# Kernel optimization log

Measured on AMD Instinct MI355X. Metric: run time of the kernel, lower is better.

Reference implementation:

```python
import jax, jax.numpy as jnp
import numpy as np

V, E, H, B, S, T = 32000, 512, 1024, 32, 64, 64

def setup_inputs() -> dict:
    key = jax.random.key(0)
    ks = jax.random.split(key, 26)
    p = 0.02  # param init scale
    inp = {
        "enc_h": jax.random.normal(ks[0], (B, S, 2 * H), dtype=jnp.float32),
        "prev_s": jax.random.normal(ks[1], (B, H), dtype=jnp.float32),
        "target": jax.random.randint(ks[2], (B, T), 0, V, dtype=jnp.int32),
        "embed": jax.random.normal(ks[3], (V, E), dtype=jnp.float32) * p,
        # Attention params
        "att_Wenc": jax.random.normal(ks[4], (2 * H, H), dtype=jnp.float32) * p,
        "att_benc": jnp.zeros((H,), dtype=jnp.float32),
        "att_Wprev": jax.random.normal(ks[5], (H, H), dtype=jnp.float32) * p,
        "att_bprev": jnp.zeros((H,), dtype=jnp.float32),
        "att_wlin": jax.random.normal(ks[6], (H, 1), dtype=jnp.float32) * p,
        "att_blin": jnp.zeros((1,), dtype=jnp.float32),
        # DecoderCell gate params (input/hidden/ctx -> 2H)
        "dc_Wi": jax.random.normal(ks[7], (E, 2 * H), dtype=jnp.float32) * p,
        "dc_bi": jnp.zeros((2 * H,), dtype=jnp.float32),
        "dc_Wh": jax.random.normal(ks[8], (H, 2 * H), dtype=jnp.float32) * p,
        "dc_bh": jnp.zeros((2 * H,), dtype=jnp.float32),
        "dc_Wc": jax.random.normal(ks[9], (2 * H, 2 * H), dtype=jnp.float32) * p,
        "dc_bc": jnp.zeros((2 * H,), dtype=jnp.float32),
        # DecoderCell candidate params (-> H)
        "dc_Wi2": jax.random.normal(ks[10], (E, H), dtype=jnp.float32) * p,
        "dc_bi2": jnp.zeros((H,), dtype=jnp.float32),
        "dc_Wh2": jax.random.normal(ks[11], (H, H), dtype=jnp.float32) * p,
        "dc_bh2": jnp.zeros((H,), dtype=jnp.float32),
        "dc_Wc2": jax.random.normal(ks[12], (2 * H, H), dtype=jnp.float32) * p,
        "dc_bc2": jnp.zeros((H,), dtype=jnp.float32),
        # dec2word
        "out_W": jax.random.normal(ks[13], (H, V), dtype=jnp.float32) * p,
        "out_b": jnp.zeros((V,), dtype=jnp.float32),
    }
    return inp


def reference(enc_h, prev_s, target, embed, att_Wenc, att_benc, att_Wprev,
              att_bprev, att_wlin, att_blin, dc_Wi, dc_bi, dc_Wh, dc_bh,
              dc_Wc, dc_bc, dc_Wi2, dc_bi2, dc_Wh2, dc_bh2, dc_Wc2, dc_bc2,
              out_W, out_b):
    h = prev_s.shape[-1]
    # Precompute attention key projection (weights fixed across timesteps)
    enc_proj = enc_h @ att_Wenc + att_benc          # B x S x H
    xs = jnp.transpose(embed[target], (1, 0, 2))    # T x B x E

    def step(s_prev, x_t):
        # Bahdanau attention
        q = s_prev @ att_Wprev + att_bprev                       # B x H
        score = jnp.tanh(enc_proj + q[:, None, :]) @ att_wlin + att_blin  # B x S x 1
        alpha = jax.nn.softmax(score[..., 0], axis=1)            # B x S (over seq)
        ctx = jnp.einsum('bs,bsh->bh', alpha, enc_h)             # B x 2H
        # GRU-like cell (original uses only the first chunk of gates)
        gates = (x_t @ dc_Wi + dc_bi) + (s_prev @ dc_Wh + dc_bh) + (ctx @ dc_Wc + dc_bc)
        reset = jax.nn.sigmoid(gates[:, :h])
        s_tilde = jnp.tanh((x_t @ dc_Wi2 + dc_bi2) + (s_prev @ dc_Wh2 + dc_bh2) + (ctx @ dc_Wc2 + dc_bc2))
        s_new = (1.0 - reset) * s_prev + reset * s_tilde
        return s_new, s_new

    final_s, dec_h = jax.lax.scan(step, prev_s, xs)   # dec_h: T x B x H
    outputs = jnp.transpose(dec_h, (1, 0, 2)) @ out_W + out_b  # B x T x V
    return outputs, final_s
```

## Files before the change

kernel.cpp:

```cpp
#include <hip/hip_runtime.h>

#define B_   32
#define S_   64
#define T_   64
#define H_   1024
#define H2_  2048
#define E_   512
#define V_   32000
#define K3_  3072
#define BT_  2048

typedef unsigned short u16;
typedef __attribute__((ext_vector_type(8))) short short8_t;
typedef __attribute__((ext_vector_type(4))) float f32x4;

__device__ __forceinline__ u16 f2bf(float f) {
  unsigned x = __float_as_uint(f);
  unsigned r = (x + 0x7fffu + ((x >> 16) & 1u)) >> 16;
  return (u16)r;
}
__device__ __forceinline__ float bf2f(u16 h) {
  return __uint_as_float(((unsigned)h) << 16);
}
__device__ __forceinline__ float frcp(float x) { return __builtin_amdgcn_rcpf(x); }
__device__ __forceinline__ float ftanh(float x) {
  float e = __expf(2.f * x);
  return 1.f - 2.f * frcp(e + 1.f);
}
__device__ __forceinline__ float fsigm(float x) {
  return frcp(1.f + __expf(-x));
}

#define KEEPV(x) asm volatile("" : "+v"(x))

__device__ __forceinline__ void st_u16(u16* p, u16 v) {
  __hip_atomic_store(p, v, __ATOMIC_RELAXED, __HIP_MEMORY_SCOPE_AGENT);
}
__device__ __forceinline__ void st_f32(float* p, float v) {
  __hip_atomic_store(p, v, __ATOMIC_RELAXED, __HIP_MEMORY_SCOPE_AGENT);
}

#define MB_ (1ull << 20)
#define KB_ (1ull << 10)
#define X_OFF    (0)
#define SPP_OFF  (0)
#define XGR_OFF  (4*MB_)
#define XG2_OFF  (12*MB_)
#define ENCT_OFF (20*MB_)
#define XCV_OFF  (20*MB_)
#define ENCP_OFF (28*MB_)
#define W2_OFF   (36*MB_)
#define WGF_OFF  (38*MB_)
#define XSV_OFF  (38*MB_)
#define DECH_OFF (46*MB_)
#define WOT_OFF  (0)
#define XS0_OFF  (62*MB_)
#define MB_OFF   (62*MB_ + 128*KB_)
#define BAR_OFF  (62*MB_ + 256*KB_)
#define WLB_OFF  (62*MB_ + 272*KB_)
#define BCR_OFF  (62*MB_ + 276*KB_)
#define BC2_OFF  (62*MB_ + 280*KB_)

__device__ __forceinline__ u16* xs_hi(char* w, int t) {
  return (u16*)(t == 0 ? (w + XS0_OFF) : (w + XSV_OFF + (size_t)(t - 1) * 131072));
}
__device__ __forceinline__ u16* xc_hi(char* w, int t) {
  return (u16*)(w + XCV_OFF + (size_t)t * 262144);
}
__device__ __forceinline__ float* spp_v(char* w, int t) {
  return (float*)(w + SPP_OFF + (size_t)t * 65536);
}

__device__ void gemm_body(char* smemRaw,
                          const float* __restrict__ A, int lda,
                          const float* __restrict__ Bm, int ldb,
                          void* __restrict__ Cv, int ldc, int outBf16,
                          const float* __restrict__ bias, const float* __restrict__ bias2,
                          int mtiles, int ntiles, int K, int bid) {
  u16 (*As)[72] = (u16(*)[72])smemRaw;
  u16 (*Bs)[72] = (u16(*)[72])(smemRaw + 128 * 72 * 2);
  int nwg = mtiles * ntiles;
  int cpx = nwg >> 3;
  int lb = (bid & 7) * cpx + (bid >> 3);
  int ntb = lb / mtiles, mtb = lb - ntb * mtiles;
  size_t m0 = (size_t)mtb * 128, n0 = (size_t)ntb * 128;
  int t = threadIdx.x, lane = t & 63, wid = t >> 6;
  int wr = (wid >> 1) * 64, wc = (wid & 1) * 64;
  f32x4 acc[4][4] = {};
  for (int k0 = 0; k0 < K; k0 += 64) {
    #pragma unroll
    for (int i = 0; i < 8; ++i) {
      int f4 = i * 256 + t;
      int row = f4 >> 4, c4 = (f4 & 15) << 2;
      float4 v = *(const float4*)(A + (m0 + row) * (size_t)lda + k0 + c4);
      ushort4 u; u.x = f2bf(v.x); u.y = f2bf(v.y); u.z = f2bf(v.z); u.w = f2bf(v.w);
      *(ushort4*)&As[row][c4] = u;
    }
    #pragma unroll
    for (int i = 0; i < 8; ++i) {
      int f4 = i * 256 + t;
      int kr = f4 >> 5, c4 = (f4 & 31) << 2;
      float4 v = *(const float4*)(Bm + (size_t)(k0 + kr) * ldb + n0 + c4);
      Bs[c4 + 0][kr] = f2bf(v.x);
      Bs[c4 + 1][kr] = f2bf(v.y);
      Bs[c4 + 2][kr] = f2bf(v.z);
      Bs[c4 + 3][kr] = f2bf(v.w);
    }
    __syncthreads();
    #pragma unroll
    for (int kk = 0; kk < 64; kk += 32) {
      int ko = kk + (lane >> 4) * 8;
      short8_t am[4], bn[4];
      #pragma unroll
      for (int m = 0; m < 4; ++m) am[m] = *(const short8_t*)&As[wr + m * 16 + (lane & 15)][ko];
      #pragma unroll
      for (int n = 0; n < 4; ++n) bn[n] = *(const short8_t*)&Bs[wc + n * 16 + (lane & 15)][ko];
      #pragma unroll
      for (int m = 0; m < 4; ++m)
        #pragma unroll
        for (int n = 0; n < 4; ++n)
          acc[m][n] = __builtin_amdgcn_mfma_f32_16x16x32_bf16(am[m], bn[n], acc[m][n], 0, 0, 0);
    }
    __syncthreads();
  }
  #pragma unroll
  for (int n = 0; n < 4; ++n) {
    int col = wc + n * 16 + (lane & 15);
    float bv = bias ? bias[n0 + col] : 0.f;
    if (bias2) bv += bias2[n0 + col];
    #pragma unroll
    for (int m = 0; m < 4; ++m) {
      size_t row = m0 + wr + m * 16 + ((lane >> 4) << 2);
      #pragma unroll
      for (int r = 0; r < 4; ++r) {
        float val = acc[m][n][r] + bv;
        if (outBf16) ((u16*)Cv)[(row + r) * (size_t)ldc + n0 + col] = f2bf(val);
        else ((float*)Cv)[(row + r) * (size_t)ldc + n0 + col] = val;
      }
    }
  }
}

__global__ __launch_bounds__(256) void k_prep(
    float* __restrict__ x, const float* __restrict__ embed, const int* __restrict__ tgt,
    u16* __restrict__ encT, const float* __restrict__ enc_h,
    u16* __restrict__ w2, const float* __restrict__ Wprev,
    u16* __restrict__ wgf, const float* __restrict__ Wh, const float* __restrict__ Wc,
    const float* __restrict__ Wh2, const float* __restrict__ Wc2,
    u16* __restrict__ encp, const float* __restrict__ Wenc,
    const float* __restrict__ benc, const float* __restrict__ bprev,
    float* __restrict__ bcr, float* __restrict__ bc2o, u16* __restrict__ wlb,
    const float* __restrict__ bi, const float* __restrict__ bh, const float* __restrict__ bc,
    const float* __restrict__ bi2, const float* __restrict__ bh2, const float* __restrict__ bc2i,
    const float* __restrict__ wlin) {
  __shared__ char pbuf[36864];
  const int bid = blockIdx.x, t = threadIdx.x;

  if (bid < 1024) {
    int f4id = bid * 256 + t;
    int row = f4id >> 7, c4 = f4id & 127;
    int tt = row >> 5, bbb = row & 31;
    int trow = tgt[bbb * T_ + tt];
    ((float4*)x)[(size_t)row * 128 + c4] = ((const float4*)embed)[(size_t)trow * 128 + c4];
  } else if (bid < 2048) {
    u16 (*ld)[68] = (u16(*)[68])pbuf;
    int teb = bid - 1024;
    int b = teb >> 5, et = teb & 31;
    int e0 = et * 64;
    #pragma unroll
    for (int i = 0; i < 4; ++i) {
      int f4 = i * 256 + t;
      int si = f4 >> 4, e4 = (f4 & 15) << 2;
      float4 v = *(const float4*)(enc_h + ((size_t)(b * 64 + si)) * H2_ + e0 + e4);
      ld[si][e4 + 0] = f2bf(v.x); ld[si][e4 + 1] = f2bf(v.y);
      ld[si][e4 + 2] = f2bf(v.z); ld[si][e4 + 3] = f2bf(v.w);
    }
    __syncthreads();
    #pragma unroll
    for (int i = 0; i < 2; ++i) {
      int idx = i * 256 + t;
      int e = idx >> 3, s8 = (idx & 7) << 3;
      short8_t o;
      #pragma unroll
      for (int k = 0; k < 8; ++k) o[k] = (short)ld[s8 + k][e];
      *(short8_t*)(encT + ((size_t)(e0 + e)) * 2048 + b * 64 + s8) = o;
    }
  } else if (bid < 2560) {
    float (*ld)[33] = (float(*)[33])pbuf;
    int pb = bid - 2048;
    int kt = pb >> 5, jt = pb & 31;
    int k0 = kt * 64, j0 = jt * 32;
    #pragma unroll
    for (int i = 0; i < 8; ++i) {
      int idx = i * 256 + t; int kr = idx >> 5, jc = idx & 31;
      ld[kr][jc] = Wprev[(size_t)(k0 + kr) * H_ + j0 + jc];
    }
    __syncthreads();
    int jloc = t >> 3, kk8 = t & 7;
    int j = j0 + jloc;
    int eg = j >> 7;
    int th = ((j & 127) << 2) | (kt >> 2);
    int i = ((kt & 3) << 3) | kk8;
    short8_t o;
    #pragma unroll
    for (int e = 0; e < 8; ++e) o[e] = (short)f2bf(ld[kk8 * 8 + e][jloc]);
    *(short8_t*)(w2 + ((size_t)((eg * 512 + th) * 32 + i)) * 8) = o;
  } else if (bid < 5632) {
    float (*ld)[33] = (float(*)[33])pbuf;
    int pgb = bid - 2560;
    int sel = pgb & 1;
    int jt  = (pgb >> 1) & 31;
    int kt  = pgb >> 6;
    int k0 = kt * 64, j0 = jt * 32;
    const float* srcW = (k0 < H_) ? (sel ? Wh2 : Wh) : (sel ? Wc2 : Wc);
    int ldw = sel ? H_ : H2_;
    int koff = (k0 < H_) ? k0 : (k0 - H_);
    #pragma unroll
    for (int i = 0; i < 8; ++i) {
      int idx = i * 256 + t; int kr = idx >> 5, jc = idx & 31;
      ld[kr][jc] = srcW[(size_t)(koff + kr) * ldw + j0 + jc];
    }
    __syncthreads();
    #pragma unroll
    for (int it = 0; it < 2; ++it) {
      int u = it * 256 + t;
      int m = u & 3, sub = (u >> 2) & 3, kbl = (u >> 4) & 1, islo = (u >> 5) & 1, gg = u >> 6;
      int jjLoc = gg * 4 + m;
      int p = 2 * (j0 + jjLoc) + sel;
      int g = p >> 3, cc = p & 7;
      int c = cc + 8 * islo;
      int KB = kt * 2 + kbl;
      size_t lin = ((size_t)(g * 96 + KB) * 4 + sub) * 16 + c;
      short8_t o;
      #pragma unroll
      for (int j = 0; j < 8; ++j) {
        float v = ld[kbl * 32 + sub * 8 + j][jjLoc];
        u16 h = f2bf(v);
        o[j] = (short)(islo ? f2bf(v - bf2f(h)) : h);
      }
      *(short8_t*)(wgf + lin * 8) = o;
    }
  } else if (bid < 5760) {
    gemm_body(pbuf, enc_h, H2_, Wenc, H_, encp, H_, 1, benc, bprev, 16, 8, H2_, bid - 5632);
  } else {
    int j = (bid - 5760) * 256 + t;
    if (j < H_) {
      bcr[j]  = bi[j]  + bh[j]  + bc[j];
      bc2o[j] = bi2[j] + bh2[j] + bc2i[j];
      wlb[j]  = f2bf(wlin[j]);
    }
  }
}

__global__ __launch_bounds__(256) void k_gemm12(
    const float* __restrict__ x,
    const float* __restrict__ Wi, const float* __restrict__ Wi2,
    float* __restrict__ xgr, float* __restrict__ xg2,
    const float* __restrict__ bcr, const float* __restrict__ bc2) {
  __shared__ char pbuf[36864];
  if (blockIdx.x < 128)
    gemm_body(pbuf, x, E_, Wi, H2_, xgr, H_, 0, bcr, nullptr, 16, 8, E_, blockIdx.x);
  else
    gemm_body(pbuf, x, E_, Wi2, H_, xg2, H_, 0, bc2, nullptr, 16, 8, E_, blockIdx.x - 128);
}

__global__ __launch_bounds__(256) void k_wtrans(u16* __restrict__ wot,
                                                const float* __restrict__ W, int nbase) {
  __shared__ u16 ld[64][68];
  int nt = blockIdx.x % 250, kt = blockIdx.x / 250;
  int n0 = nbase + nt * 64, k0 = kt * 64;
  int t = threadIdx.x;
  #pragma unroll
  for (int i = 0; i < 4; ++i) {
    int f4 = i * 256 + t;
    int kr = f4 >> 4, n4 = (f4 & 15) << 2;
    float4 v = *(const float4*)(W + (size_t)(k0 + kr) * V_ + n0 + n4);
    ld[kr][n4 + 0] = f2bf(v.x); ld[kr][n4 + 1] = f2bf(v.y);
    ld[kr][n4 + 2] = f2bf(v.z); ld[kr][n4 + 3] = f2bf(v.w);
  }
  __syncthreads();
  #pragma unroll
  for (int i = 0; i < 2; ++i) {
    int idx = i * 256 + t;
    int n = idx >> 3, k8 = (idx & 7) << 3;
    short8_t o;
    #pragma unroll
    for (int k = 0; k < 8; ++k) o[k] = (short)ld[k8 + k][n];
    *(short8_t*)(wot + ((size_t)(nt * 64 + n)) * H_ + k0 + k8) = o;
  }
}

__global__ __launch_bounds__(256) void k_gemm2(
    const u16* __restrict__ A, const u16* __restrict__ Bt,
    float* __restrict__ C, const float* __restrict__ bias, int n0g) {
  __shared__ u16 As[128][72];
  __shared__ u16 Bs[128][72];
  int bid = blockIdx.x;
  int lb = (bid & 7) * 250 + (bid >> 3);
  int mtb = lb & 15, ntb = lb >> 4;
  size_t m0 = (size_t)mtb * 128;
  size_t nl0 = (size_t)ntb * 128;
  int t = threadIdx.x, lane = t & 63, wid = t >> 6;
  int wr = (wid >> 1) * 64, wc = (wid & 1) * 64;
  f32x4 acc[4][4] = {};
  for (int k0 = 0; k0 < H_; k0 += 64) {
    #pragma unroll
    for (int i = 0; i < 4; ++i) {
      int idx = i * 256 + t;
      int row = idx >> 3, c8 = (idx & 7) << 3;
      *(short8_t*)&As[row][c8] = *(const short8_t*)(A + (m0 + row) * H_ + k0 + c8);
      *(short8_t*)&Bs[row][c8] = *(const short8_t*)(Bt + (nl0 + row) * H_ + k0 + c8);
    }
    __syncthreads();
    #pragma unroll
    for (int kk = 0; kk < 64; kk += 32) {
      int ko = kk + (lane >> 4) * 8;
      short8_t am[4], bn[4];
      #pragma unroll
      for (int m = 0; m < 4; ++m) am[m] = *(const short8_t*)&As[wr + m * 16 + (lane & 15)][ko];
      #pragma unroll
      for (int n = 0; n < 4; ++n) bn[n] = *(const short8_t*)&Bs[wc + n * 16 + (lane & 15)][ko];
      #pragma unroll
      for (int m = 0; m < 4; ++m)
        #pragma unroll
        for (int n = 0; n < 4; ++n)
          acc[m][n] = __builtin_amdgcn_mfma_f32_16x16x32_bf16(am[m], bn[n], acc[m][n], 0, 0, 0);
    }
    __syncthreads();
  }
  #pragma unroll
  for (int n = 0; n < 4; ++n) {
    int col = n0g + (int)nl0 + wc + n * 16 + (lane & 15);
    float bv = bias[col];
    #pragma unroll
    for (int m = 0; m < 4; ++m) {
      size_t row = m0 + wr + m * 16 + ((lane >> 4) << 2);
      #pragma unroll
      for (int r = 0; r < 4; ++r)
        C[(row + r) * (size_t)V_ + col] = acc[m][n][r] + bv;
    }
  }
}


__device__ __forceinline__ void gridbar(int* bar, int target) {
  asm volatile("s_waitcnt vmcnt(0)" ::: "memory");
  __syncthreads();
  if (threadIdx.x == 0) {
    int* leafcnt = bar;
    int* root    = bar + 512;
    int* leafep  = bar + 768;
    int li = blockIdx.x >> 3;
    if (__hip_atomic_fetch_add(&leafcnt[li * 16], 1, __ATOMIC_RELAXED, __HIP_MEMORY_SCOPE_AGENT) == 7) {
      __hip_atomic_store(&leafcnt[li * 16], 0, __ATOMIC_RELAXED, __HIP_MEMORY_SCOPE_AGENT);
      if (__hip_atomic_fetch_add(root, 1, __ATOMIC_RELAXED, __HIP_MEMORY_SCOPE_AGENT) == 31) {
        __hip_atomic_store(root, 0, __ATOMIC_RELAXED, __HIP_MEMORY_SCOPE_AGENT);
        #pragma unroll
        for (int i = 0; i < 32; ++i)
          __hip_atomic_store(&leafep[i * 16], target, __ATOMIC_RELAXED, __HIP_MEMORY_SCOPE_AGENT);
      }
    }
    while (__hip_atomic_load(&leafep[li * 16], __ATOMIC_RELAXED, __HIP_MEMORY_SCOPE_AGENT) != target)
      __builtin_amdgcn_s_sleep(2);
  }
  __syncthreads();
}

#define MFMA16(a, b, c) __builtin_amdgcn_mfma_f32_16x16x32_bf16((a), (b), (c), 0, 0, 0)

__global__ __launch_bounds__(512, 1) void k_mega(
    char* w, u16* __restrict__ dech, float* __restrict__ fout,
    const u16* __restrict__ w2, const u16* __restrict__ wgf,
    const u16* __restrict__ encp, const u16* __restrict__ encT,
    const float* __restrict__ xgr, const float* __restrict__ xg2,
    const float* __restrict__ prev_s, const u16* __restrict__ wlb,
    int* bar, int* mb) {
  const int t = threadIdx.x, blk = blockIdx.x;
  const int lane = t & 63, wid = t >> 6;
  const int l15 = lane & 15, l4 = lane >> 4;
  const int klo = l4 * 8;
  __shared__ short8_t wg_lds[6144];
  __shared__ f32x4 scr[1024];
  __shared__ float sc[64];
  __shared__ u16 sL[1024];
  __shared__ float qL[8 * 17];
  int ep = 0;

  for (int i = t; i < 6144; i += 512)
    wg_lds[i] = *(const short8_t*)(wgf + ((size_t)blk * 6144 + i) * 8);

  const int bb = blk >> 3, eg = blk & 7;

  const int si_a = t >> 3, jg = t & 7;
  short8_t epv2[2], wlv2[2];
  {
    const u16* p = encp + ((size_t)(bb * 64 + si_a)) * H_ + eg * 128 + jg * 16;
    epv2[0] = *(const short8_t*)(p);     KEEPV(epv2[0]);
    epv2[1] = *(const short8_t*)(p + 8); KEEPV(epv2[1]);
    const u16* q = wlb + eg * 128 + jg * 16;
    wlv2[0] = *(const short8_t*)(q);     KEEPV(wlv2[0]);
    wlv2[1] = *(const short8_t*)(q + 8); KEEPV(wlv2[1]);
  }
  const int eloc = t >> 1, half = t & 1;
  const int ecol = eg * 256 + eloc;
  short8_t et[4];
  #pragma unroll
  for (int i = 0; i < 4; ++i) {
    et[i] = *(const short8_t*)(encT + (size_t)ecol * 2048 + bb * 64 + half * 32 + i * 8);
    KEEPV(et[i]);
  }

  const int pc4 = blk * 8 + l15, jcol = pc4 >> 1, isc = pc4 & 1;
  const int rb = wid * 16 + l4 * 4;
  const bool fin = (wid < 2) && (l15 < 8);
  float sreg[4] = {0.f, 0.f, 0.f, 0.f};

  {
    int idx = blk * 512 + t;
    u16* xs0h = xs_hi(w, 0);
    u16* xs0l = xs0h + B_ * H_;
    if (idx < B_ * H_) {
      float v = prev_s[idx];
      u16 h = f2bf(v);
      st_u16(&xs0h[idx], h);
      st_u16(&xs0l[idx], f2bf(v - bf2f(h)));
    }
    if (fin) {
      #pragma unroll
      for (int r = 0; r < 4; ++r) sreg[r] = prev_s[(rb + r) * H_ + jcol];
    }
  }
  gridbar(bar, ++ep);

  for (int ts = 0; ts < T_; ++ts) {
    const u16* xsh = xs_hi(w, ts);
    const u16* xsl = xsh + B_ * H_;
    u16* xch = xc_hi(w, ts);
    u16* xcl = xch + B_ * H2_;
    float* spp = spp_v(w, ts);
    int* mbp = mb + (ts * 32 + bb) * 16;

    if (t < 128)
      *(short8_t*)&sL[t * 8] = *(const short8_t*)(xsh + bb * H_ + t * 8);
    float xv[4] = {0.f, 0.f, 0.f, 0.f};
    if (fin) {
      const float* xg = isc ? xg2 : xgr;
      #pragma unroll
      for (int r = 0; r < 4; ++r)
        xv[r] = xg[((size_t)ts * B_ + rb + r) * H_ + jcol];
    }
    short8_t pA[4], pB[4], loA[4], loB[4];
    #pragma unroll
    for (int i = 0; i < 4; ++i) {
      int k = (wid + 8 * i) * 32 + klo;
      pA[i]  = *(const short8_t*)(xsh + l15 * H_ + k);        KEEPV(pA[i]);
      pB[i]  = *(const short8_t*)(xsh + (l15 + 16) * H_ + k); KEEPV(pB[i]);
      loA[i] = *(const short8_t*)(xsl + l15 * H_ + k);        KEEPV(loA[i]);
      loB[i] = *(const short8_t*)(xsl + (l15 + 16) * H_ + k); KEEPV(loB[i]);
    }
    __syncthreads();

    {
      const int rot = (t & 3) * 2;
      float qa = 0.f;
      const u16* wp = w2 + ((size_t)(eg * 512 + t)) * 256;
      const u16* sp = sL + (t & 3) * 256;
      #pragma unroll
      for (int i = 0; i < 32; ++i) {
        int ii = (i + rot) & 31;
        short8_t wv = *(const short8_t*)(wp + ii * 8);
        short8_t sv = *(const short8_t*)(sp + ii * 8);
        #pragma unroll
        for (int e = 0; e < 8; ++e)
          qa += bf2f((u16)wv[e]) * bf2f((u16)sv[e]);
      }
      qa += __shfl_xor(qa, 1, 64);
      qa += __shfl_xor(qa, 2, 64);
      if ((t & 3) == 0) { int j = t >> 2; qL[(j >> 4) * 17 + (j & 15)] = qa; }
    }
    __syncthreads();

    {
      float p = 0.f;
      #pragma unroll
      for (int jj = 0; jj < 16; ++jj) {
        float qv = qL[jg * 17 + jj];
        p += ftanh(bf2f((u16)epv2[jj >> 3][jj & 7]) + qv) * bf2f((u16)wlv2[jj >> 3][jj & 7]);
      }
      p += __shfl_xor(p, 1, 64);
      p += __shfl_xor(p, 2, 64);
      p += __shfl_xor(p, 4, 64);
      if (jg == 0) st_f32(&spp[(bb * 64 + si_a) * 8 + eg], p);
    }
    asm volatile("s_waitcnt vmcnt(0)" ::: "memory");
    __syncthreads();
    if (t == 0)
      __hip_atomic_fetch_add(mbp, 1, __ATOMIC_RELAXED, __HIP_MEMORY_SCOPE_AGENT);

    f32x4 aA = {}, aB = {};
    #pragma unroll
    for (int i = 0; i < 4; ++i) {
      short8_t bv = wg_lds[(wid + 8 * i) * 64 + lane];
      aA = MFMA16(pA[i],  bv, aA);
      aB = MFMA16(pB[i],  bv, aB);
      aA = MFMA16(loA[i], bv, aA);
      aB = MFMA16(loB[i], bv, aB);
    }

    if (t == 0) {
      while (__hip_atomic_load(mbp, __ATOMIC_RELAXED, __HIP_MEMORY_SCOPE_AGENT) != 8)
        __builtin_amdgcn_s_sleep(1);
    }
    __syncthreads();

    if (wid == 0) {
      const float* pp = spp + ((size_t)(bb * 64 + lane)) * 8;
      float4 a0 = *(const float4*)(pp);
      float4 a1 = *(const float4*)(pp + 4);
      float v = (a0.x + a0.y + a0.z + a0.w) + (a1.x + a1.y + a1.z + a1.w);
      float m = v;
      #pragma unroll
      for (int off = 32; off; off >>= 1) m = fmaxf(m, __shfl_xor(m, off, 64));
      float e = __expf(v - m);
      float s = e;
      #pragma unroll
      for (int off = 32; off; off >>= 1) s += __shfl_xor(s, off, 64);
      sc[lane] = e * frcp(s);
    }
    __syncthreads();
    {
      float a = 0.f;
      #pragma unroll
      for (int i = 0; i < 4; ++i)
        #pragma unroll
        for (int j = 0; j < 8; ++j)
          a += sc[half * 32 + i * 8 + j] * bf2f((u16)et[i][j]);
      a += __shfl_xor(a, 1, 64);
      if (half == 0) {
        u16 hh = f2bf(a);
        st_u16(&xch[bb * H2_ + ecol], hh);
        st_u16(&xcl[bb * H2_ + ecol], f2bf(a - bf2f(hh)));
      }
    }
    gridbar(bar, ++ep);

    {
      #pragma unroll
      for (int i = 4; i < 12; ++i) {
        int kb = wid + 8 * i;
        int k = kb * 32 + klo - H_;
        short8_t hA = *(const short8_t*)(xch + l15 * H2_ + k);
        short8_t lA = *(const short8_t*)(xcl + l15 * H2_ + k);
        short8_t hB = *(const short8_t*)(xch + (l15 + 16) * H2_ + k);
        short8_t lB = *(const short8_t*)(xcl + (l15 + 16) * H2_ + k);
        short8_t bv = wg_lds[kb * 64 + lane];
        aA = MFMA16(hA, bv, aA);
        aA = MFMA16(lA, bv, aA);
        aB = MFMA16(hB, bv, aB);
        aB = MFMA16(lB, bv, aB);
      }
      scr[(wid * 2 + 0) * 64 + lane] = aA;
      scr[(wid * 2 + 1) * 64 + lane] = aB;
      __syncthreads();
      if (wid < 2) {
        f32x4 s = scr[wid * 64 + lane];
        #pragma unroll
        for (int i = 1; i < 8; ++i) s += scr[(i * 2 + wid) * 64 + lane];
        float tot[4];
        #pragma unroll
        for (int r = 0; r < 4; ++r) tot[r] = s[r] + __shfl_xor(s[r], 8, 64);
        if (l15 < 8) {
          u16* nsh = xs_hi(w, ts + 1);
          u16* nsl = nsh + B_ * H_;
          #pragma unroll
          for (int r = 0; r < 4; ++r) {
            int brow = rb + r;
            float pre = tot[r] + xv[r];
            float mate = __shfl_xor(pre, 1, 64);
            float rpre = isc ? mate : pre;
            float cpre = isc ? pre : mate;
            float rg = fsigm(rpre);
            float cg = ftanh(cpre);
            float sp = sreg[r];
            float sn = sp + rg * (cg - sp);
            sreg[r] = sn;
            if (!isc) {
              u16 hh = f2bf(sn);
              st_u16(&nsh[brow * H_ + jcol], hh);
              st_u16(&nsl[brow * H_ + jcol], f2bf(sn - bf2f(hh)));
              dech[((size_t)brow * T_ + ts) * H_ + jcol] = hh;
              if (ts == T_ - 1) fout[brow * H_ + jcol] = sn;
            }
          }
        }
      }
    }
    gridbar(bar, ++ep);
  }
}


extern "C" void kernel_launch(void* const* d_in, const int* in_sizes, int n_in,
                              void* d_out, int out_size, void* d_ws, size_t ws_size,
                              hipStream_t stream) {
  const float* enc_h    = (const float*)d_in[0];
  const float* prev_s   = (const float*)d_in[1];
  const int*   target   = (const int*)d_in[2];
  const float* embed    = (const float*)d_in[3];
  const float* att_Wenc = (const float*)d_in[4];
  const float* att_benc = (const float*)d_in[5];
  const float* att_Wprev= (const float*)d_in[6];
  const float* att_bprev= (const float*)d_in[7];
  const float* att_wlin = (const float*)d_in[8];
  const float* dc_Wi    = (const float*)d_in[10];
  const float* dc_bi    = (const float*)d_in[11];
  const float* dc_Wh    = (const float*)d_in[12];
  const float* dc_bh    = (const float*)d_in[13];
  const float* dc_Wc    = (const float*)d_in[14];
  const float* dc_bc    = (const float*)d_in[15];
  const float* dc_Wi2   = (const float*)d_in[16];
  const float* dc_bi2   = (const float*)d_in[17];
  const float* dc_Wh2   = (const float*)d_in[18];
  const float* dc_bh2   = (const float*)d_in[19];
  const float* dc_Wc2   = (const float*)d_in[20];
  const float* dc_bc2   = (const float*)d_in[21];
  const float* out_W    = (const float*)d_in[22];
  const float* out_b    = (const float*)d_in[23];

  char* w = (char*)d_ws;
  float* x    = (float*)(w + X_OFF);
  float* xgr  = (float*)(w + XGR_OFF);
  float* xg2  = (float*)(w + XG2_OFF);
  u16*  encT  = (u16*)(w + ENCT_OFF);
  u16*  encp  = (u16*)(w + ENCP_OFF);
  u16*  w2    = (u16*)(w + W2_OFF);
  u16*  wgf   = (u16*)(w + WGF_OFF);
  u16*  wot   = (u16*)(w + WOT_OFF);
  u16*  dech  = (u16*)(w + DECH_OFF);
  u16*  wlb   = (u16*)(w + WLB_OFF);
  float* bcr  = (float*)(w + BCR_OFF);
  float* bc2  = (float*)(w + BC2_OFF);
  int*  bar   = (int*)(w + BAR_OFF);
  int*  mb    = (int*)(w + MB_OFF);
  float* fout = (float*)d_out + (size_t)BT_ * V_;

  hipMemsetAsync(w + MB_OFF, 0, 136 * KB_, stream);

  k_prep<<<5764, 256, 0, stream>>>(x, embed, target, encT, enc_h,
                                   w2, att_Wprev, wgf, dc_Wh, dc_Wc, dc_Wh2, dc_Wc2,
                                   encp, att_Wenc, att_benc, att_bprev,
                                   bcr, bc2, wlb,
                                   dc_bi, dc_bh, dc_bc, dc_bi2, dc_bh2, dc_bc2, att_wlin);
  k_gemm12<<<256, 256, 0, stream>>>(x, dc_Wi, dc_Wi2, xgr, xg2, bcr, bc2);

  k_mega<<<256, 512, 0, stream>>>(w, dech, fout,
                                  w2, wgf, encp, encT, xgr, xg2,
                                  prev_s, wlb, bar, mb);

  k_wtrans<<<4000, 256, 0, stream>>>(wot, out_W, 0);
  k_gemm2 <<<2000, 256, 0, stream>>>(dech, wot, (float*)d_out, out_b, 0);
  k_wtrans<<<4000, 256, 0, stream>>>(wot, out_W, 16000);
  k_gemm2 <<<2000, 256, 0, stream>>>(dech, wot, (float*)d_out, out_b, 16000);
}
```

Baseline: 2.799 ms.

## Fuse output weight transpose and bf16 conversion into vocab GEMM

Removes the separate weight transpose/convert kernels and the bf16 staging buffer, having the output GEMM load fp32 out_W tiles directly, convert to bf16 and transpose through LDS before MFMA. This eliminates a large intermediate write and read and several launches, but each M-tile now re-reads fp32 weights, doubling per-tile weight bytes and adding an LDS transpose stage and extra barrier per k-step. Also skips the final grid barrier after the last recurrent step.

```diff
diff --git a/kernel.cpp b/kernel.cpp
--- a/kernel.cpp
+++ b/kernel.cpp
@@ -53,7 +53,6 @@
 #define WGF_OFF  (38*MB_)
 #define XSV_OFF  (38*MB_)
 #define DECH_OFF (46*MB_)
-#define WOT_OFF  (0)
 #define XS0_OFF  (62*MB_)
 #define MB_OFF   (62*MB_ + 128*KB_)
 #define BAR_OFF  (62*MB_ + 256*KB_)
@@ -264,42 +263,17 @@
     gemm_body(pbuf, x, E_, Wi2, H_, xg2, H_, 0, bc2, nullptr, 16, 8, E_, blockIdx.x - 128);
 }
 
-__global__ __launch_bounds__(256) void k_wtrans(u16* __restrict__ wot,
-                                                const float* __restrict__ W, int nbase) {
-  __shared__ u16 ld[64][68];
-  int nt = blockIdx.x % 250, kt = blockIdx.x / 250;
-  int n0 = nbase + nt * 64, k0 = kt * 64;
-  int t = threadIdx.x;
-  #pragma unroll
-  for (int i = 0; i < 4; ++i) {
-    int f4 = i * 256 + t;
-    int kr = f4 >> 4, n4 = (f4 & 15) << 2;
-    float4 v = *(const float4*)(W + (size_t)(k0 + kr) * V_ + n0 + n4);
-    ld[kr][n4 + 0] = f2bf(v.x); ld[kr][n4 + 1] = f2bf(v.y);
-    ld[kr][n4 + 2] = f2bf(v.z); ld[kr][n4 + 3] = f2bf(v.w);
-  }
-  __syncthreads();
-  #pragma unroll
-  for (int i = 0; i < 2; ++i) {
-    int idx = i * 256 + t;
-    int n = idx >> 3, k8 = (idx & 7) << 3;
-    short8_t o;
-    #pragma unroll
-    for (int k = 0; k < 8; ++k) o[k] = (short)ld[k8 + k][n];
-    *(short8_t*)(wot + ((size_t)(nt * 64 + n)) * H_ + k0 + k8) = o;
-  }
-}
-
-__global__ __launch_bounds__(256) void k_gemm2(
-    const u16* __restrict__ A, const u16* __restrict__ Bt,
-    float* __restrict__ C, const float* __restrict__ bias, int n0g) {
+__global__ __launch_bounds__(256) void k_gemm2d(
+    const u16* __restrict__ A, const float* __restrict__ W,
+    float* __restrict__ C, const float* __restrict__ bias) {
   __shared__ u16 As[128][72];
   __shared__ u16 Bs[128][72];
+  __shared__ u16 Bstage[64 * 132];
   int bid = blockIdx.x;
-  int lb = (bid & 7) * 250 + (bid >> 3);
+  int lb = (bid & 7) * 500 + (bid >> 3);
   int mtb = lb & 15, ntb = lb >> 4;
   size_t m0 = (size_t)mtb * 128;
-  size_t nl0 = (size_t)ntb * 128;
+  size_t n0 = (size_t)ntb * 128;
   int t = threadIdx.x, lane = t & 63, wid = t >> 6;
   int wr = (wid >> 1) * 64, wc = (wid & 1) * 64;
   f32x4 acc[4][4] = {};
@@ -309,7 +283,24 @@
       int idx = i * 256 + t;
       int row = idx >> 3, c8 = (idx & 7) << 3;
       *(short8_t*)&As[row][c8] = *(const short8_t*)(A + (m0 + row) * H_ + k0 + c8);
-      *(short8_t*)&Bs[row][c8] = *(const short8_t*)(Bt + (nl0 + row) * H_ + k0 + c8);
+    }
+    #pragma unroll
+    for (int i = 0; i < 8; ++i) {
+      int f4 = i * 256 + t;
+      int kr = f4 >> 5, c4 = (f4 & 31) << 2;
+      float4 v = *(const float4*)(W + (size_t)(k0 + kr) * V_ + n0 + c4);
+      ushort4 u; u.x = f2bf(v.x); u.y = f2bf(v.y); u.z = f2bf(v.z); u.w = f2bf(v.w);
+      *(ushort4*)&Bstage[kr * 132 + c4] = u;
+    }
+    __syncthreads();
+    #pragma unroll
+    for (int i = 0; i < 4; ++i) {
+      int jj = i * 256 + t;
+      int n = jj & 127, k8 = jj >> 7;
+      short8_t o;
+      #pragma unroll
+      for (int e = 0; e < 8; ++e) o[e] = (short)Bstage[(k8 * 8 + e) * 132 + n];
+      *(short8_t*)&Bs[n][k8 * 8] = o;
     }
     __syncthreads();
     #pragma unroll
@@ -330,7 +321,7 @@
   }
   #pragma unroll
   for (int n = 0; n < 4; ++n) {
-    int col = n0g + (int)nl0 + wc + n * 16 + (lane & 15);
+    int col = (int)n0 + wc + n * 16 + (lane & 15);
     float bv = bias[col];
     #pragma unroll
     for (int m = 0; m < 4; ++m) {
@@ -595,7 +586,7 @@
         }
       }
     }
-    gridbar(bar, ++ep);
+    if (ts != T_ - 1) gridbar(bar, ++ep);
   }
 }
 
@@ -635,7 +626,6 @@
   u16*  encp  = (u16*)(w + ENCP_OFF);
   u16*  w2    = (u16*)(w + W2_OFF);
   u16*  wgf   = (u16*)(w + WGF_OFF);
-  u16*  wot   = (u16*)(w + WOT_OFF);
   u16*  dech  = (u16*)(w + DECH_OFF);
   u16*  wlb   = (u16*)(w + WLB_OFF);
   float* bcr  = (float*)(w + BCR_OFF);
@@ -657,8 +647,5 @@
                                   w2, wgf, encp, encT, xgr, xg2,
                                   prev_s, wlb, bar, mb);
 
-  k_wtrans<<<4000, 256, 0, stream>>>(wot, out_W, 0);
-  k_gemm2 <<<2000, 256, 0, stream>>>(dech, wot, (float*)d_out, out_b, 0);
-  k_wtrans<<<4000, 256, 0, stream>>>(wot, out_W, 16000);
-  k_gemm2 <<<2000, 256, 0, stream>>>(dech, wot, (float*)d_out, out_b, 16000);
-}
+  k_gemm2d<<<4000, 256, 0, stream>>>(dech, out_W, (float*)d_out, out_b);
+}
```

Result: slower. 2.894 ms (+3.4%).
